# Performance work log

Measured on AMD Instinct MI355X. Metric: run time of the kernel, lower is better.

The kernel has to match this reference:

```python
import jax, jax.numpy as jnp
import numpy as np
from functools import partial

B, T, D, H, V, L, NL = 2, 2048, 512, 8, 32000, 4, 3
HID = 4 * D
HD = D // H
EPS = 1e-5


def layernorm(x, g, b):
    mu = jnp.mean(x, axis=-1, keepdims=True)
    var = jnp.mean(jnp.square(x - mu), axis=-1, keepdims=True)
    return (x - mu) * jax.lax.rsqrt(var + EPS) * g + b


def self_mod_attn(x, Wq, Wk, Wv, Wo):
    # x: [B,T,D]; W*: [D,D] (applied as x @ W)
    def heads(w):
        return jnp.transpose((x @ w).reshape(B, T, H, HD), (1, 0, 2, 3))  # [T,B,H,HD]
    q, k, v = heads(Wq), heads(Wk), heads(Wv)

    def step(mem, qkv):
        q_t, k_t, v_t = qkv  # each [B,H,HD]
        mem = mem + jnp.einsum('bhd,bhk->hdk', v_t, k_t) / B  # batch-mean outer product
        y_t = jnp.einsum('hdk,bhk->bhd', mem, q_t)
        return mem, y_t

    mem0 = jnp.zeros((H, HD, HD), dtype=x.dtype)
    _, ys = jax.lax.scan(step, mem0, (q, k, v))  # ys: [T,B,H,HD]
    out = jnp.transpose(ys, (1, 0, 2, 3)).reshape(B, T, D)
    return out @ Wo


def cms(x, W1, b1, W2, b2):
    # Continuum memory system: NL parallel MLP levels (dim -> 4*dim -> dim, GELU), averaged.
    h = jax.nn.gelu(jnp.einsum('btd,ndh->nbth', x, W1) + b1[:, None, None, :])
    y = jnp.einsum('nbth,nhd->nbtd', h, W2) + b2[:, None, None, :]
    return jnp.mean(y, axis=0)


def setup_inputs() -> dict:
    key = jax.random.key(0)
    ks = jax.random.split(key, 16)
    std = 0.02
    p = {
        'emb': jax.random.normal(ks[0], (V, D), jnp.float32) * std,
        'pos': jax.random.normal(ks[1], (2048, D), jnp.float32) * std,
        'ln1_g': jnp.ones((L, D)), 'ln1_b': jnp.zeros((L, D)),
        'Wq': jax.random.normal(ks[2], (L, D, D), jnp.float32) * std,
        'Wk': jax.random.normal(ks[3], (L, D, D), jnp.float32) * std,
        'Wv': jax.random.normal(ks[4], (L, D, D), jnp.float32) * std,
        'Wo': jax.random.normal(ks[5], (L, D, D), jnp.float32) * std,
        'ln2_g': jnp.ones((L, D)), 'ln2_b': jnp.zeros((L, D)),
        'cms_W1': jax.random.normal(ks[6], (L, NL, D, HID), jnp.float32) * std,
        'cms_b1': jnp.zeros((L, NL, HID)),
        'cms_W2': jax.random.normal(ks[7], (L, NL, HID, D), jnp.float32) * std,
        'cms_b2': jnp.zeros((L, NL, D)),
        'lnf_g': jnp.ones((D,)), 'lnf_b': jnp.zeros((D,)),
        'input_ids': jax.random.randint(ks[8], (B, T), 0, V, jnp.int32),
    }
    return p


def reference(emb, pos, ln1_g, ln1_b, Wq, Wk, Wv, Wo, ln2_g, ln2_b,
              cms_W1, cms_b1, cms_W2, cms_b2, lnf_g, lnf_b, input_ids):
    x = emb[input_ids] + pos[:T][None, :, :]  # [B,T,D]
    for l in range(L):
        x = x + self_mod_attn(layernorm(x, ln1_g[l], ln1_b[l]), Wq[l], Wk[l], Wv[l], Wo[l])
        x = x + cms(layernorm(x, ln2_g[l], ln2_b[l]), cms_W1[l], cms_b1[l], cms_W2[l], cms_b2[l])
    x = layernorm(x, lnf_g, lnf_b)
    logits = x @ emb.T  # tied head, [B,T,V]
    return logits
```

## Files before the change

### kernel.cpp

```cpp
#include <hip/hip_runtime.h>
#include <stdint.h>

#define B_ 2
#define T_ 2048
#define D_ 512
#define H_ 8
#define HD_ 64
#define V_ 32000
#define L_ 4
#define NL_ 3
#define HID_ 2048
#define NROW 4096
#define CCH 64
#define CROWS 128
#define NC 32
#define EPS_ 1e-5f

typedef __attribute__((ext_vector_type(8))) __bf16 bf16x8;
typedef __attribute__((ext_vector_type(4))) float f32x4;

__device__ __forceinline__ float b2f(unsigned short u) {
  union { uint32_t i; float f; } v; v.i = ((uint32_t)u) << 16; return v.f;
}
__device__ __forceinline__ unsigned short f2b(float f) {
  union { float f; uint32_t i; } v; v.f = f;
  uint32_t u = v.i;
  u += 0x7fffu + ((u >> 16) & 1u);
  return (unsigned short)(u >> 16);
}

__global__ __launch_bounds__(256) void k_prep(
    const float* __restrict__ emb, const float* __restrict__ pos,
    const int* __restrict__ ids,
    const float* __restrict__ Wq, const float* __restrict__ Wk,
    const float* __restrict__ Wv, const float* __restrict__ Wo,
    const float* __restrict__ W1, const float* __restrict__ W2,
    const float* __restrict__ b2,
    const float* __restrict__ ln1g, const float* __restrict__ ln1b,
    unsigned short* __restrict__ WqkvT, unsigned short* __restrict__ WoT,
    unsigned short* __restrict__ W1T, unsigned short* __restrict__ W2cat,
    unsigned short* __restrict__ embB, float* __restrict__ bsum,
    float* __restrict__ x, unsigned short* __restrict__ h) {
  int bid = blockIdx.x, tid = threadIdx.x;
  __shared__ float tile[32][33];
  __shared__ float red[4], red2[4];
  int tx = tid & 31, ty = tid >> 5;
  if (bid < 4096) {
    int z = bid >> 8, r = bid & 255;
    int bx = (r & 15) * 32, by = (r >> 4) * 32;
    const float* in; unsigned short* out;
    if (z < 12) {
      int l = z / 3, m = z - l * 3;
      in = (m == 0 ? Wq : m == 1 ? Wk : Wv) + (size_t)l * D_ * D_;
      out = WqkvT + (size_t)z * D_ * D_;
    } else {
      in = Wo + (size_t)(z - 12) * D_ * D_;
      out = WoT + (size_t)(z - 12) * D_ * D_;
    }
#pragma unroll
    for (int i = 0; i < 4; i++)
      tile[ty + 8 * i][tx] = in[(size_t)(by + ty + 8 * i) * D_ + bx + tx];
    __syncthreads();
#pragma unroll
    for (int i = 0; i < 4; i++)
      out[(size_t)(bx + ty + 8 * i) * D_ + by + tx] = f2b(tile[tx][ty + 8 * i]);
  } else if (bid < 16384) {
    int s = bid - 4096;
    int z = s >> 10, r = s & 1023;
    int bx = (r & 63) * 32, by = (r >> 6) * 32;
    const float* in = W1 + (size_t)z * D_ * HID_;
    unsigned short* out = W1T + (size_t)z * HID_ * D_;
#pragma unroll
    for (int i = 0; i < 4; i++)
      tile[ty + 8 * i][tx] = in[(size_t)(by + ty + 8 * i) * HID_ + bx + tx];
    __syncthreads();
#pragma unroll
    for (int i = 0; i < 4; i++)
      out[(size_t)(bx + ty + 8 * i) * D_ + by + tx] = f2b(tile[tx][ty + 8 * i]);
  } else if (bid < 28672) {
    int s = bid - 16384;
    int z = s >> 10, r = s & 1023;
    int l = z / 3, n = z - l * 3;
    int bx = (r & 15) * 32, by = (r >> 4) * 32;
    const float* in = W2 + (size_t)z * HID_ * D_;
#pragma unroll
    for (int i = 0; i < 4; i++)
      tile[ty + 8 * i][tx] = in[(size_t)(by + ty + 8 * i) * D_ + bx + tx];
    __syncthreads();
#pragma unroll
    for (int i = 0; i < 4; i++)
      W2cat[((size_t)l * D_ + bx + ty + 8 * i) * (NL_ * HID_) + n * HID_ + by + tx] =
          f2b(tile[tx][ty + 8 * i]);
  } else if (bid < 44672) {
    int s = bid - 28672;
    int base = (s * 256 + tid) * 4;
    float4 v = *(const float4*)(emb + base);
    unsigned short o[4] = { f2b(v.x), f2b(v.y), f2b(v.z), f2b(v.w) };
    *(uint2*)(embB + base) = *(const uint2*)o;
  } else if (bid < 46720) {
    int s = bid - 44672;
    int i = s * 256 + tid;
    int row = i >> 7, cg = i & 127;
    int t = row & (T_ - 1);
    int id = ids[row];
    float4 e = ((const float4*)(emb + (size_t)id * D_))[cg];
    float4 p = ((const float4*)(pos + (size_t)t * D_))[cg];
    float4 xv; xv.x = e.x + p.x; xv.y = e.y + p.y; xv.z = e.z + p.z; xv.w = e.w + p.w;
    ((float4*)(x + (size_t)row * D_))[cg] = xv;
    float sum = xv.x + xv.y + xv.z + xv.w;
#pragma unroll
    for (int o = 32; o >= 1; o >>= 1) sum += __shfl_xor(sum, o);
    int wv = tid >> 6;
    if ((tid & 63) == 0) red[wv] = sum;
    __syncthreads();
    int wb = (tid >> 7) * 2;
    float mu = (red[wb] + red[wb + 1]) * (1.f / D_);
    float dx = xv.x - mu, dy = xv.y - mu, dz = xv.z - mu, dw = xv.w - mu;
    float s2 = dx * dx + dy * dy + dz * dz + dw * dw;
#pragma unroll
    for (int o = 32; o >= 1; o >>= 1) s2 += __shfl_xor(s2, o);
    if ((tid & 63) == 0) red2[wv] = s2;
    __syncthreads();
    float var = (red2[wb] + red2[wb + 1]) * (1.f / D_);
    float rs = rsqrtf(var + EPS_);
    float4 gv = ((const float4*)ln1g)[cg];
    float4 bv = ((const float4*)ln1b)[cg];
    unsigned short o4[4] = { f2b(dx * rs * gv.x + bv.x), f2b(dy * rs * gv.y + bv.y),
                             f2b(dz * rs * gv.z + bv.z), f2b(dw * rs * gv.w + bv.w) };
    *(uint2*)(h + (size_t)row * D_ + cg * 4) = *(const uint2*)o4;
  } else {
    int s = bid - 46720;
    int l = s >> 1, d = (s & 1) * 256 + tid;
    float acc = 0.f;
#pragma unroll
    for (int n = 0; n < NL_; n++) acc += b2[((size_t)l * NL_ + n) * D_ + d];
    bsum[(size_t)l * D_ + d] = acc;
  }
}

__global__ __launch_bounds__(128) void k_ln(
    const float* __restrict__ x, const float* __restrict__ g,
    const float* __restrict__ b, unsigned short* __restrict__ out) {
  int row = blockIdx.x;
  int tid = threadIdx.x;
  const float* xr = x + (size_t)row * D_;
  float4 v = ((const float4*)xr)[tid];
  float s = v.x + v.y + v.z + v.w;
#pragma unroll
  for (int o = 32; o >= 1; o >>= 1) s += __shfl_xor(s, o);
  __shared__ float red[2], red2[2];
  int wv = tid >> 6;
  if ((tid & 63) == 0) red[wv] = s;
  __syncthreads();
  float mu = (red[0] + red[1]) * (1.f / D_);
  float dx = v.x - mu, dy = v.y - mu, dz = v.z - mu, dw = v.w - mu;
  float s2 = dx * dx + dy * dy + dz * dz + dw * dw;
#pragma unroll
  for (int o = 32; o >= 1; o >>= 1) s2 += __shfl_xor(s2, o);
  if ((tid & 63) == 0) red2[wv] = s2;
  __syncthreads();
  float var = (red2[0] + red2[1]) * (1.f / D_);
  float rs = rsqrtf(var + EPS_);
  float4 gv = ((const float4*)g)[tid];
  float4 bv = ((const float4*)b)[tid];
  unsigned short o4[4] = { f2b(dx * rs * gv.x + bv.x), f2b(dy * rs * gv.y + bv.y),
                           f2b(dz * rs * gv.z + bv.z), f2b(dw * rs * gv.w + bv.w) };
  *(uint2*)(out + (size_t)row * D_ + tid * 4) = *(const uint2*)o4;
}

__global__ __launch_bounds__(256) void k_cmsred_ln(
    float* __restrict__ x, const float* __restrict__ parts,
    const float* __restrict__ bsum, const float* __restrict__ g,
    const float* __restrict__ b, unsigned short* __restrict__ h) {
  int bid = blockIdx.x, tid = threadIdx.x;
  int row = bid * 2 + (tid >> 7);
  int cg = tid & 127;
  size_t base = (size_t)row * D_ + cg * 4;
  float4 xv = *(const float4*)(x + base);
  float4 p0 = *(const float4*)(parts + base);
  float4 p1 = *(const float4*)(parts + (size_t)NROW * D_ + base);
  float4 p2 = *(const float4*)(parts + 2ull * NROW * D_ + base);
  float4 bs = *(const float4*)(bsum + cg * 4);
  const float k3 = 1.f / 3.f;
  xv.x += (p0.x + p1.x + p2.x + bs.x) * k3;
  xv.y += (p0.y + p1.y + p2.y + bs.y) * k3;
  xv.z += (p0.z + p1.z + p2.z + bs.z) * k3;
  xv.w += (p0.w + p1.w + p2.w + bs.w) * k3;
  *(float4*)(x + base) = xv;
  float sum = xv.x + xv.y + xv.z + xv.w;
#pragma unroll
  for (int o = 32; o >= 1; o >>= 1) sum += __shfl_xor(sum, o);
  __shared__ float red[4], red2[4];
  int wv = tid >> 6;
  if ((tid & 63) == 0) red[wv] = sum;
  __syncthreads();
  int wb = (tid >> 7) * 2;
  float mu = (red[wb] + red[wb + 1]) * (1.f / D_);
  float dx = xv.x - mu, dy = xv.y - mu, dz = xv.z - mu, dw = xv.w - mu;
  float s2 = dx * dx + dy * dy + dz * dz + dw * dw;
#pragma unroll
  for (int o = 32; o >= 1; o >>= 1) s2 += __shfl_xor(s2, o);
  if ((tid & 63) == 0) red2[wv] = s2;
  __syncthreads();
  float var = (red2[wb] + red2[wb + 1]) * (1.f / D_);
  float rs = rsqrtf(var + EPS_);
  float4 gv = ((const float4*)g)[cg];
  float4 bv = ((const float4*)b)[cg];
  unsigned short o4[4] = { f2b(dx * rs * gv.x + bv.x), f2b(dy * rs * gv.y + bv.y),
                           f2b(dz * rs * gv.z + bv.z), f2b(dw * rs * gv.w + bv.w) };
  *(uint2*)(h + base) = *(const uint2*)o4;
}

enum { E_QKV = 0, E_RES = 1, E_GELU = 2, E_PART = 3, E_F32 = 4 };

template <int TR, int NW>
__device__ __forceinline__ void stage_tile(
    const unsigned short* __restrict__ gbase, int ldk, unsigned short* lds,
    int wave, int lane) {
#pragma unroll
  for (int q = 0; q < 4; q++) {
    int Lb = (q * NW + wave) << 10;
    int L = Lb + lane * 16;
    int row = L >> 7;
    int colb = (L & 127) ^ ((row & 7) << 4);
    const unsigned short* gsrc = gbase + (size_t)row * ldk + (colb >> 1);
    __builtin_amdgcn_global_load_lds(
        (const __attribute__((address_space(1))) uint32_t*)gsrc,
        (__attribute__((address_space(3))) uint32_t*)(lds + (Lb >> 1)),
        16, 0, 0);
  }
}

template <int EPI>
__global__ __launch_bounds__(256, 2) void k_gemm128(
    const unsigned short* __restrict__ A,
    const unsigned short* __restrict__ Bt,
    const float* __restrict__ bias,
    void* __restrict__ Out,
    int Kext, int ldk, int N, int ldOut) {
  int z = blockIdx.z;
  A  += (size_t)z * Kext;
  Bt += (size_t)z * Kext;
  int lane = threadIdx.x & 63, wave = threadIdx.x >> 6;
  int wm = wave >> 1, wn = wave & 1;
  int bx = blockIdx.x, by = blockIdx.y;

  __shared__ __align__(16) unsigned short As[2][128 * 64];
  __shared__ __align__(16) unsigned short Bs[2][128 * 64];

  const unsigned short* Ab = A + (size_t)by * 128 * ldk;
  const unsigned short* Bb = Bt + (size_t)bx * 128 * ldk;

  f32x4 acc[4][4] = {};
  int nk = Kext / 64;
  stage_tile<128, 4>(Ab, ldk, As[0], wave, lane);
  stage_tile<128, 4>(Bb, ldk, Bs[0], wave, lane);
  __syncthreads();
  for (int kt = 0; kt < nk; kt++) {
    int cur = kt & 1;
    if (kt + 1 < nk) {
      stage_tile<128, 4>(Ab + (size_t)(kt + 1) * 64, ldk, As[cur ^ 1], wave, lane);
      stage_tile<128, 4>(Bb + (size_t)(kt + 1) * 64, ldk, Bs[cur ^ 1], wave, lane);
    }
    const char* Ac = (const char*)As[cur];
    const char* Bc = (const char*)Bs[cur];
#pragma unroll
    for (int kk = 0; kk < 2; kk++) {
      bf16x8 af[4], bfr[4];
#pragma unroll
      for (int mt = 0; mt < 4; mt++) {
        int row = wm * 64 + mt * 16 + (lane & 15);
        int off = ((row << 7) | (kk * 64 + ((lane >> 4) << 4))) ^ ((row & 7) << 4);
        af[mt] = *(const bf16x8*)(Ac + off);
      }
#pragma unroll
      for (int nt = 0; nt < 4; nt++) {
        int row = wn * 64 + nt * 16 + (lane & 15);
        int off = ((row << 7) | (kk * 64 + ((lane >> 4) << 4))) ^ ((row & 7) << 4);
        bfr[nt] = *(const bf16x8*)(Bc + off);
      }
#pragma unroll
      for (int mt = 0; mt < 4; mt++)
#pragma unroll
        for (int nt = 0; nt < 4; nt++)
          acc[mt][nt] = __builtin_amdgcn_mfma_f32_16x16x32_bf16(
              af[mt], bfr[nt], acc[mt][nt], 0, 0, 0);
    }
    __syncthreads();
  }

  int gm = by * 128 + wm * 64;
  int gn = bx * 128 + wn * 64;
#pragma unroll
  for (int mt = 0; mt < 4; mt++) {
#pragma unroll
    for (int nt = 0; nt < 4; nt++) {
      int m0 = gm + mt * 16 + ((lane >> 4) << 2);
      int n = gn + nt * 16 + (lane & 15);
#pragma unroll
      for (int j = 0; j < 4; j++) {
        float v = acc[mt][nt][j];
        int m = m0 + j;
        if constexpr (EPI == E_QKV) {
          int zq = n >> 9, col = n & 511;
          ((unsigned short*)Out)[((size_t)zq * NROW + m) * D_ + col] = f2b(v);
        } else if constexpr (EPI == E_RES) {
          size_t idx = (size_t)m * ldOut + n;
          ((float*)Out)[idx] = bias[idx] + v;
        } else if constexpr (EPI == E_GELU) {
          size_t idx = (size_t)m * ldOut + n;
          v += bias[n];
          float u2 = 1.5957691216057308f * (v + 0.044715f * v * v * v);
          float sg = 1.f / (1.f + __expf(-u2));
          ((unsigned short*)Out)[idx] = f2b(v * sg);
        } else {
          ((float*)Out)[(size_t)z * NROW * D_ + (size_t)m * ldOut + n] = v;
        }
      }
    }
  }
}

__global__ __launch_bounds__(512) void k_gemm256(
    const unsigned short* __restrict__ A,
    const unsigned short* __restrict__ Bt,
    void* __restrict__ Out,
    int K, int N, int ldOut) {
  int lane = threadIdx.x & 63, wave = threadIdx.x >> 6;
  int wm = wave >> 2, wn = wave & 3;
  int lin = blockIdx.y * 125 + blockIdx.x;
  int seg = lin / 400, rem = lin % 400;
  int bx = seg * 25 + rem % 25, by = rem / 25;

  __shared__ __align__(16) unsigned short As[256 * 64];
  __shared__ __align__(16) unsigned short Bs[256 * 64];

  const unsigned short* Ab = A + (size_t)by * 256 * K;
  const unsigned short* Bb = Bt + (size_t)bx * 256 * K;

  f32x4 acc[8][4] = {};
  int nk = K / 64;
  for (int kt = 0; kt < nk; kt++) {
    stage_tile<256, 8>(Ab + (size_t)kt * 64, K, As, wave, lane);
    stage_tile<256, 8>(Bb + (size_t)kt * 64, K, Bs, wave, lane);
    __syncthreads();
    const char* Ac = (const char*)As;
    const char* Bc = (const char*)Bs;
#pragma unroll
    for (int kk = 0; kk < 2; kk++) {
      bf16x8 af[8], bfr[4];
#pragma unroll
      for (int mt = 0; mt < 8; mt++) {
        int row = wm * 128 + mt * 16 + (lane & 15);
        int off = ((row << 7) | (kk * 64 + ((lane >> 4) << 4))) ^ ((row & 7) << 4);
        af[mt] = *(const bf16x8*)(Ac + off);
      }
#pragma unroll
      for (int nt = 0; nt < 4; nt++) {
        int row = wn * 64 + nt * 16 + (lane & 15);
        int off = ((row << 7) | (kk * 64 + ((lane >> 4) << 4))) ^ ((row & 7) << 4);
        bfr[nt] = *(const bf16x8*)(Bc + off);
      }
#pragma unroll
      for (int mt = 0; mt < 8; mt++)
#pragma unroll
        for (int nt = 0; nt < 4; nt++)
          acc[mt][nt] = __builtin_amdgcn_mfma_f32_16x16x32_bf16(
              af[mt], bfr[nt], acc[mt][nt], 0, 0, 0);
    }
    __syncthreads();
  }

  int gm = by * 256 + wm * 128;
  int gn = bx * 256 + wn * 64;
#pragma unroll
  for (int mt = 0; mt < 8; mt++) {
#pragma unroll
    for (int nt = 0; nt < 4; nt++) {
      int m0 = gm + mt * 16 + ((lane >> 4) << 2);
      int n = gn + nt * 16 + (lane & 15);
#pragma unroll
      for (int j = 0; j < 4; j++)
        ((float*)Out)[(size_t)(m0 + j) * ldOut + n] = acc[mt][nt][j];
    }
  }
}

__device__ __forceinline__ void unpack8f(uint4 u, float* dst) {
  dst[0] = b2f((unsigned short)(u.x & 0xffff)); dst[1] = b2f((unsigned short)(u.x >> 16));
  dst[2] = b2f((unsigned short)(u.y & 0xffff)); dst[3] = b2f((unsigned short)(u.y >> 16));
  dst[4] = b2f((unsigned short)(u.z & 0xffff)); dst[5] = b2f((unsigned short)(u.z >> 16));
  dst[6] = b2f((unsigned short)(u.w & 0xffff)); dst[7] = b2f((unsigned short)(u.w >> 16));
}

__global__ __launch_bounds__(256) void k_attnA(
    const unsigned short* __restrict__ kbuf, const unsigned short* __restrict__ vbuf,
    float* __restrict__ G) {
  int c = blockIdx.x, h = blockIdx.y;
  __shared__ __align__(16) float Ks[CROWS][HD_];
  __shared__ __align__(16) float Vs[CROWS][HD_];
  int tid = threadIdx.x;
#pragma unroll
  for (int it = 0; it < 4; it++) {
    int gi = it * 256 + tid;
    int r = gi >> 3, c8 = gi & 7;
    int bb = r & 1, tt = c * CCH + (r >> 1);
    size_t goff = ((size_t)bb * T_ + tt) * D_ + h * HD_ + c8 * 8;
    uint4 kv = *(const uint4*)(kbuf + goff);
    uint4 vv = *(const uint4*)(vbuf + goff);
    unpack8f(kv, &Ks[r][c8 * 8]);
    unpack8f(vv, &Vs[r][c8 * 8]);
  }
  __syncthreads();
  int d = tid & 63, kb = (tid >> 6) * 16;
  float acc[16] = {};
  for (int r = 0; r < CROWS; r++) {
    float vd = Vs[r][d];
#pragma unroll
    for (int j = 0; j < 16; j++) acc[j] += vd * Ks[r][kb + j];
  }
  float* Gp = G + (((size_t)c * H_ + h) * HD_ + d) * HD_ + kb;
#pragma unroll
  for (int j = 0; j < 16; j++) Gp[j] = 0.5f * acc[j];
}

__global__ __launch_bounds__(256) void k_attnB(const float* __restrict__ G,
                                               float* __restrict__ Mem) {
  int hh = blockIdx.x >> 4, seg = blockIdx.x & 15;
  int idx = seg * 256 + threadIdx.x;
  float g[NC];
#pragma unroll
  for (int c = 0; c < NC; c++)
    g[c] = G[((size_t)c * H_ + hh) * (HD_ * HD_) + idx];
  float m = 0.f;
#pragma unroll
  for (int c = 0; c < NC; c++) {
    Mem[((size_t)c * H_ + hh) * (HD_ * HD_) + idx] = m;
    m += g[c];
  }
}

__global__ __launch_bounds__(256) void k_attnC(
    const unsigned short* __restrict__ qbuf, const unsigned short* __restrict__ kbuf,
    const unsigned short* __restrict__ vbuf, const float* __restrict__ Mem,
    unsigned short* __restrict__ ybuf) {
  int c = blockIdx.x, h = blockIdx.y;
  __shared__ __align__(16) unsigned short smem[32768];
  unsigned short* Qs  = smem;
  unsigned short* Ksh = smem + 8192;
  unsigned short* Vt  = smem + 16384;
  unsigned short* Mhi = smem + 24576;
  unsigned short* Mlo = smem + 28672;
  unsigned short* Ps  = smem;

  int tid = threadIdx.x, lane = tid & 63, w = tid >> 6;
#pragma unroll
  for (int it = 0; it < 4; it++) {
    int gi = it * 256 + tid;
    int r = gi >> 3, g8 = gi & 7;
    int bb = r & 1, tt = c * CCH + (r >> 1);
    size_t go = ((size_t)bb * T_ + tt) * D_ + h * HD_ + g8 * 8;
    int qc = (g8 * 8) ^ ((r & 7) << 3);
    *(uint4*)(Qs + r * 64 + qc) = *(const uint4*)(qbuf + go);
    *(uint4*)(Ksh + r * 64 + qc) = *(const uint4*)(kbuf + go);
    uint4 vv = *(const uint4*)(vbuf + go);
    const unsigned short* vp = (const unsigned short*)&vv;
#pragma unroll
    for (int j = 0; j < 8; j++) {
      int d = g8 * 8 + j;
      int t = (d & 7) ^ (d >> 3);
      Vt[d * 128 + (r ^ (t << 3))] = vp[j];
    }
  }
  {
    const float* Mp = Mem + (((size_t)c * H_ + h) << 12);
#pragma unroll
    for (int it = 0; it < 16; it++) {
      int i = it * 256 + tid;
      int d = i >> 6, k = i & 63;
      float m = Mp[i];
      unsigned short hi = f2b(m);
      float lo = m - b2f(hi);
      int col = k ^ ((d & 7) << 3);
      Mhi[d * 64 + col] = hi;
      Mlo[d * 64 + col] = f2b(lo);
    }
  }
  __syncthreads();

  int row0 = w * 32;
  f32x4 sacc[2][8] = {};
  f32x4 yacc[2][4] = {};
#pragma unroll
  for (int kk = 0; kk < 2; kk++) {
    bf16x8 aq[2];
#pragma unroll
    for (int mt = 0; mt < 2; mt++) {
      int row = row0 + mt * 16 + (lane & 15);
      aq[mt] = *(const bf16x8*)(Qs + row * 64 +
                ((kk * 32 + ((lane >> 4) << 3)) ^ ((row & 7) << 3)));
    }
#pragma unroll
    for (int nt = 0; nt < 8; nt++) {
      int row = nt * 16 + (lane & 15);
      bf16x8 bk = *(const bf16x8*)(Ksh + row * 64 +
                ((kk * 32 + ((lane >> 4) << 3)) ^ ((row & 7) << 3)));
#pragma unroll
      for (int mt = 0; mt < 2; mt++)
        sacc[mt][nt] = __builtin_amdgcn_mfma_f32_16x16x32_bf16(aq[mt], bk,
                                                               sacc[mt][nt], 0, 0, 0);
    }
#pragma unroll
    for (int nt = 0; nt < 4; nt++) {
      int row = nt * 16 + (lane & 15);
      int off = row * 64 + ((kk * 32 + ((lane >> 4) << 3)) ^ ((row & 7) << 3));
      bf16x8 bh = *(const bf16x8*)(Mhi + off);
      bf16x8 bl = *(const bf16x8*)(Mlo + off);
#pragma unroll
      for (int mt = 0; mt < 2; mt++) {
        yacc[mt][nt] = __builtin_amdgcn_mfma_f32_16x16x32_bf16(aq[mt], bh,
                                                               yacc[mt][nt], 0, 0, 0);
        yacc[mt][nt] = __builtin_amdgcn_mfma_f32_16x16x32_bf16(aq[mt], bl,
                                                               yacc[mt][nt], 0, 0, 0);
      }
    }
  }
  __syncthreads();

#pragma unroll
  for (int mt = 0; mt < 2; mt++)
#pragma unroll
    for (int nt = 0; nt < 8; nt++)
#pragma unroll
      for (int j = 0; j < 4; j++) {
        int qr = row0 + mt * 16 + ((lane >> 4) << 2) + j;
        int ks = nt * 16 + (lane & 15);
        float v = ((ks >> 1) <= (qr >> 1)) ? sacc[mt][nt][j] * 0.5f : 0.f;
        Ps[qr * 128 + (ks ^ ((qr & 7) << 3))] = f2b(v);
      }
  __syncthreads();

  for (int kb = 0; kb <= w; kb++) {
    bf16x8 ap[2];
#pragma unroll
    for (int mt = 0; mt < 2; mt++) {
      int row = row0 + mt * 16 + (lane & 15);
      ap[mt] = *(const bf16x8*)(Ps + row * 128 +
                ((kb * 32 + ((lane >> 4) << 3)) ^ ((row & 7) << 3)));
    }
#pragma unroll
    for (int nt = 0; nt < 4; nt++) {
      int d = nt * 16 + (lane & 15);
      int t = (d & 7) ^ (d >> 3);
      int gb = (kb * 32 + ((lane >> 4) << 3)) ^ (t << 3);
      bf16x8 bv = *(const bf16x8*)(Vt + d * 128 + gb);
#pragma unroll
      for (int mt = 0; mt < 2; mt++)
        yacc[mt][nt] = __builtin_amdgcn_mfma_f32_16x16x32_bf16(ap[mt], bv,
                                                               yacc[mt][nt], 0, 0, 0);
    }
  }

#pragma unroll
  for (int mt = 0; mt < 2; mt++)
#pragma unroll
    for (int nt = 0; nt < 4; nt++)
#pragma unroll
      for (int j = 0; j < 4; j++) {
        int qr = row0 + mt * 16 + ((lane >> 4) << 2) + j;
        int d = nt * 16 + (lane & 15);
        int bb = qr & 1, tl = qr >> 1;
        ybuf[((size_t)bb * T_ + c * CCH + tl) * D_ + h * HD_ + d] =
            f2b(yacc[mt][nt][j]);
      }
}

extern "C" void kernel_launch(void* const* d_in, const int* in_sizes, int n_in,
                              void* d_out, int out_size, void* d_ws, size_t ws_size,
                              hipStream_t stream) {
  (void)in_sizes; (void)n_in; (void)out_size; (void)ws_size;
  const float* emb  = (const float*)d_in[0];
  const float* pos  = (const float*)d_in[1];
  const float* ln1g = (const float*)d_in[2];
  const float* ln1b = (const float*)d_in[3];
  const float* Wq   = (const float*)d_in[4];
  const float* Wk   = (const float*)d_in[5];
  const float* Wv   = (const float*)d_in[6];
  const float* Wo   = (const float*)d_in[7];
  const float* ln2g = (const float*)d_in[8];
  const float* ln2b = (const float*)d_in[9];
  const float* W1   = (const float*)d_in[10];
  const float* b1   = (const float*)d_in[11];
  const float* W2   = (const float*)d_in[12];
  const float* b2   = (const float*)d_in[13];
  const float* lnfg = (const float*)d_in[14];
  const float* lnfb = (const float*)d_in[15];
  const int*   ids  = (const int*)d_in[16];

  char* w = (char*)d_ws;
  size_t off = 0;
  auto alloc = [&](size_t bytes) -> void* {
    void* p = w + off; off += (bytes + 255) & ~(size_t)255; return p;
  };
  const size_t DD = (size_t)D_ * D_;
  unsigned short* WqkvT = (unsigned short*)alloc(12ull * DD * 2);
  unsigned short* WoT   = (unsigned short*)alloc(4ull * DD * 2);
  unsigned short* W1T   = (unsigned short*)alloc((size_t)L_ * NL_ * HID_ * D_ * 2);
  unsigned short* W2cat = (unsigned short*)alloc((size_t)L_ * D_ * NL_ * HID_ * 2);
  unsigned short* embB  = (unsigned short*)alloc((size_t)V_ * D_ * 2);
  float* bsum           = (float*)alloc((size_t)L_ * D_ * 4);
  float* x              = (float*)alloc((size_t)NROW * D_ * 4);
  unsigned short* h     = (unsigned short*)alloc((size_t)NROW * D_ * 2);
  unsigned short* qkv   = (unsigned short*)alloc(3ull * NROW * D_ * 2);
  unsigned short* ybuf  = (unsigned short*)alloc((size_t)NROW * D_ * 2);
  float* G              = (float*)alloc((size_t)NC * H_ * HD_ * HD_ * 4);
  float* Mem            = (float*)alloc((size_t)NC * H_ * HD_ * HD_ * 4);
  float* parts          = (float*)qkv;
  unsigned short* hmid  = (unsigned short*)alloc((size_t)NROW * NL_ * HID_ * 2);

  dim3 blk(256);
  k_prep<<<dim3(46728), blk, 0, stream>>>(emb, pos, ids, Wq, Wk, Wv, Wo, W1, W2, b2,
                                          ln1g, ln1b,
                                          WqkvT, WoT, W1T, W2cat, embB, bsum, x, h);

  unsigned short* qb = qkv;
  unsigned short* kb = qkv + (size_t)NROW * D_;
  unsigned short* vb = qkv + 2ull * NROW * D_;

  for (int l = 0; l < L_; l++) {
    k_gemm128<E_QKV><<<dim3(12, 32), blk, 0, stream>>>(
        h, WqkvT + (size_t)l * 3 * DD, bsum, qkv, D_, D_, 3 * D_, D_);
    k_attnA<<<dim3(NC, H_), blk, 0, stream>>>(kb, vb, G);
    k_attnB<<<dim3(H_ * 16), blk, 0, stream>>>(G, Mem);
    k_attnC<<<dim3(NC, H_), blk, 0, stream>>>(qb, kb, vb, Mem, ybuf);
    k_gemm128<E_RES><<<dim3(4, 32), blk, 0, stream>>>(
        ybuf, WoT + (size_t)l * DD, x, x, D_, D_, D_, D_);
    k_ln<<<dim3(NROW), dim3(128), 0, stream>>>(x, ln2g + l * D_, ln2b + l * D_, h);
    k_gemm128<E_GELU><<<dim3(48, 32), blk, 0, stream>>>(
        h, W1T + (size_t)l * NL_ * HID_ * D_, b1 + (size_t)l * NL_ * HID_, hmid,
        D_, D_, NL_ * HID_, NL_ * HID_);
    k_gemm128<E_PART><<<dim3(4, 32, 3), blk, 0, stream>>>(
        hmid, W2cat + (size_t)l * D_ * NL_ * HID_, bsum, parts,
        2048, NL_ * HID_, D_, D_);
    const float* gn = (l < 3) ? (ln1g + (l + 1) * D_) : lnfg;
    const float* bn = (l < 3) ? (ln1b + (l + 1) * D_) : lnfb;
    k_cmsred_ln<<<dim3(NROW / 2), blk, 0, stream>>>(x, parts, bsum + l * D_, gn, bn, h);
  }
  k_gemm256<<<dim3(125, 16), dim3(512), 0, stream>>>(h, embB, d_out, D_, V_, V_);
}
```

Baseline: 919.2 us.

## Double-buffer 256-tile GEMM, use it for GELU GEMM, fold prefix-sum into attnC

The 256x256 GEMM now double-buffers its LDS tiles so the global loads for the next K-slice overlap the MFMA work on the current one. It is templated and also used for the CMS up-projection with the GELU epilogue, replacing the 128-tile kernel there. The separate prefix-sum kernel (attnB) is removed and each attnC block sums the earlier chunk outer products itself, saving a launch and the Mem round trip at the cost of redundant reads. attnA's inner loop is also rewritten to use float4 LDS reads; doubled LDS lowers occupancy to one block per CU.

Result: slower. 972.8 us (+5.8%).

```diff
diff --git a/kernel.cpp b/kernel.cpp
--- a/kernel.cpp
+++ b/kernel.cpp
@@ -307,81 +307,95 @@
         } else if constexpr (EPI == E_RES) {
           size_t idx = (size_t)m * ldOut + n;
           ((float*)Out)[idx] = bias[idx] + v;
-        } else if constexpr (EPI == E_GELU) {
-          size_t idx = (size_t)m * ldOut + n;
+        } else {
+          ((float*)Out)[(size_t)z * NROW * D_ + (size_t)m * ldOut + n] = v;
+        }
+      }
+    }
+  }
+}
+
+template <int EPI>
+__global__ __launch_bounds__(512, 1) void k_gemm256(
+    const unsigned short* __restrict__ A,
+    const unsigned short* __restrict__ Bt,
+    const float* __restrict__ bias,
+    void* __restrict__ Out,
+    int K, int N, int ldOut) {
+  int lane = threadIdx.x & 63, wave = threadIdx.x >> 6;
+  int wm = wave >> 2, wn = wave & 3;
+  int bx = blockIdx.x, by = blockIdx.y;
+  if constexpr (EPI == E_F32) {
+    int lin = blockIdx.y * 125 + blockIdx.x;
+    int seg = lin / 400, rem = lin % 400;
+    bx = seg * 25 + rem % 25;  by = rem / 25;
+  }
+
+  __shared__ __align__(16) unsigned short As[2][256 * 64];
+  __shared__ __align__(16) unsigned short Bs[2][256 * 64];
+
+  const unsigned short* Ab = A + (size_t)by * 256 * K;
+  const unsigned short* Bb = Bt + (size_t)bx * 256 * K;
+
+  f32x4 acc[8][4] = {};
+  int nk = K / 64;
+  stage_tile<256, 8>(Ab, K, As[0], wave, lane);
+  stage_tile<256, 8>(Bb, K, Bs[0], wave, lane);
+  __syncthreads();
+  for (int kt = 0; kt < nk; kt++) {
+    int cur = kt & 1;
+    if (kt + 1 < nk) {
+      stage_tile<256, 8>(Ab + (size_t)(kt + 1) * 64, K, As[cur ^ 1], wave, lane);
+      stage_tile<256, 8>(Bb + (size_t)(kt + 1) * 64, K, Bs[cur ^ 1], wave, lane);
+    }
+    const char* Ac = (const char*)As[cur];
+    const char* Bc = (const char*)Bs[cur];
+#pragma unroll
+    for (int kk = 0; kk < 2; kk++) {
+      bf16x8 af[8], bfr[4];
+#pragma unroll
+      for (int mt = 0; mt < 8; mt++) {
+        int row = wm * 128 + mt * 16 + (lane & 15);
+        int off = ((row << 7) | (kk * 64 + ((lane >> 4) << 4))) ^ ((row & 7) << 4);
+        af[mt] = *(const bf16x8*)(Ac + off);
+      }
+#pragma unroll
+      for (int nt = 0; nt < 4; nt++) {
+        int row = wn * 64 + nt * 16 + (lane & 15);
+        int off = ((row << 7) | (kk * 64 + ((lane >> 4) << 4))) ^ ((row & 7) << 4);
+        bfr[nt] = *(const bf16x8*)(Bc + off);
+      }
+#pragma unroll
+      for (int mt = 0; mt < 8; mt++)
+#pragma unroll
+        for (int nt = 0; nt < 4; nt++)
+          acc[mt][nt] = __builtin_amdgcn_mfma_f32_16x16x32_bf16(
+              af[mt], bfr[nt], acc[mt][nt], 0, 0, 0);
+    }
+    __syncthreads();
+  }
+
+  int gm = by * 256 + wm * 128;
+  int gn = bx * 256 + wn * 64;
+#pragma unroll
+  for (int mt = 0; mt < 8; mt++) {
+#pragma unroll
+    for (int nt = 0; nt < 4; nt++) {
+      int m0 = gm + mt * 16 + ((lane >> 4) << 2);
+      int n = gn + nt * 16 + (lane & 15);
+#pragma unroll
+      for (int j = 0; j < 4; j++) {
+        float v = acc[mt][nt][j];
+        size_t idx = (size_t)(m0 + j) * ldOut + n;
+        if constexpr (EPI == E_GELU) {
           v += bias[n];
           float u2 = 1.5957691216057308f * (v + 0.044715f * v * v * v);
           float sg = 1.f / (1.f + __expf(-u2));
           ((unsigned short*)Out)[idx] = f2b(v * sg);
         } else {
-          ((float*)Out)[(size_t)z * NROW * D_ + (size_t)m * ldOut + n] = v;
+          ((float*)Out)[idx] = v;
         }
       }
-    }
-  }
-}
-
-__global__ __launch_bounds__(512) void k_gemm256(
-    const unsigned short* __restrict__ A,
-    const unsigned short* __restrict__ Bt,
-    void* __restrict__ Out,
-    int K, int N, int ldOut) {
-  int lane = threadIdx.x & 63, wave = threadIdx.x >> 6;
-  int wm = wave >> 2, wn = wave & 3;
-  int lin = blockIdx.y * 125 + blockIdx.x;
-  int seg = lin / 400, rem = lin % 400;
-  int bx = seg * 25 + rem % 25, by = rem / 25;
-
-  __shared__ __align__(16) unsigned short As[256 * 64];
-  __shared__ __align__(16) unsigned short Bs[256 * 64];
-
-  const unsigned short* Ab = A + (size_t)by * 256 * K;
-  const unsigned short* Bb = Bt + (size_t)bx * 256 * K;
-
-  f32x4 acc[8][4] = {};
-  int nk = K / 64;
-  for (int kt = 0; kt < nk; kt++) {
-    stage_tile<256, 8>(Ab + (size_t)kt * 64, K, As, wave, lane);
-    stage_tile<256, 8>(Bb + (size_t)kt * 64, K, Bs, wave, lane);
-    __syncthreads();
-    const char* Ac = (const char*)As;
-    const char* Bc = (const char*)Bs;
-#pragma unroll
-    for (int kk = 0; kk < 2; kk++) {
-      bf16x8 af[8], bfr[4];
-#pragma unroll
-      for (int mt = 0; mt < 8; mt++) {
-        int row = wm * 128 + mt * 16 + (lane & 15);
-        int off = ((row << 7) | (kk * 64 + ((lane >> 4) << 4))) ^ ((row & 7) << 4);
-        af[mt] = *(const bf16x8*)(Ac + off);
-      }
-#pragma unroll
-      for (int nt = 0; nt < 4; nt++) {
-        int row = wn * 64 + nt * 16 + (lane & 15);
-        int off = ((row << 7) | (kk * 64 + ((lane >> 4) << 4))) ^ ((row & 7) << 4);
-        bfr[nt] = *(const bf16x8*)(Bc + off);
-      }
-#pragma unroll
-      for (int mt = 0; mt < 8; mt++)
-#pragma unroll
-        for (int nt = 0; nt < 4; nt++)
-          acc[mt][nt] = __builtin_amdgcn_mfma_f32_16x16x32_bf16(
-              af[mt], bfr[nt], acc[mt][nt], 0, 0, 0);
-    }
-    __syncthreads();
-  }
-
-  int gm = by * 256 + wm * 128;
-  int gn = bx * 256 + wn * 64;
-#pragma unroll
-  for (int mt = 0; mt < 8; mt++) {
-#pragma unroll
-    for (int nt = 0; nt < 4; nt++) {
-      int m0 = gm + mt * 16 + ((lane >> 4) << 2);
-      int n = gn + nt * 16 + (lane & 15);
-#pragma unroll
-      for (int j = 0; j < 4; j++)
-        ((float*)Out)[(size_t)(m0 + j) * ldOut + n] = acc[mt][nt][j];
     }
   }
 }
@@ -416,33 +430,21 @@
   float acc[16] = {};
   for (int r = 0; r < CROWS; r++) {
     float vd = Vs[r][d];
-#pragma unroll
-    for (int j = 0; j < 16; j++) acc[j] += vd * Ks[r][kb + j];
+    const float4* Kr = (const float4*)(&Ks[r][kb]);
+    float4 k0 = Kr[0], k1 = Kr[1], k2 = Kr[2], k3 = Kr[3];
+    acc[0] += vd * k0.x;  acc[1] += vd * k0.y;  acc[2] += vd * k0.z;  acc[3] += vd * k0.w;
+    acc[4] += vd * k1.x;  acc[5] += vd * k1.y;  acc[6] += vd * k1.z;  acc[7] += vd * k1.w;
+    acc[8] += vd * k2.x;  acc[9] += vd * k2.y;  acc[10] += vd * k2.z; acc[11] += vd * k2.w;
+    acc[12] += vd * k3.x; acc[13] += vd * k3.y; acc[14] += vd * k3.z; acc[15] += vd * k3.w;
   }
   float* Gp = G + (((size_t)c * H_ + h) * HD_ + d) * HD_ + kb;
 #pragma unroll
   for (int j = 0; j < 16; j++) Gp[j] = 0.5f * acc[j];
-}
-
-__global__ __launch_bounds__(256) void k_attnB(const float* __restrict__ G,
-                                               float* __restrict__ Mem) {
-  int hh = blockIdx.x >> 4, seg = blockIdx.x & 15;
-  int idx = seg * 256 + threadIdx.x;
-  float g[NC];
-#pragma unroll
-  for (int c = 0; c < NC; c++)
-    g[c] = G[((size_t)c * H_ + hh) * (HD_ * HD_) + idx];
-  float m = 0.f;
-#pragma unroll
-  for (int c = 0; c < NC; c++) {
-    Mem[((size_t)c * H_ + hh) * (HD_ * HD_) + idx] = m;
-    m += g[c];
-  }
 }
 
 __global__ __launch_bounds__(256) void k_attnC(
     const unsigned short* __restrict__ qbuf, const unsigned short* __restrict__ kbuf,
-    const unsigned short* __restrict__ vbuf, const float* __restrict__ Mem,
+    const unsigned short* __restrict__ vbuf, const float* __restrict__ G,
     unsigned short* __restrict__ ybuf) {
   int c = blockIdx.x, h = blockIdx.y;
   __shared__ __align__(16) unsigned short smem[32768];
@@ -454,6 +456,18 @@
   unsigned short* Ps  = smem;
 
   int tid = threadIdx.x, lane = tid & 63, w = tid >> 6;
+  float macc[16] = {};
+  for (int cp = 0; cp < c; cp++) {
+    const float4* gp = (const float4*)(G + ((size_t)cp * H_ + h) * (HD_ * HD_)) + tid * 4;
+#pragma unroll
+    for (int j4 = 0; j4 < 4; j4++) {
+      float4 gv = gp[j4];
+      macc[j4 * 4]     += gv.x;
+      macc[j4 * 4 + 1] += gv.y;
+      macc[j4 * 4 + 2] += gv.z;
+      macc[j4 * 4 + 3] += gv.w;
+    }
+  }
 #pragma unroll
   for (int it = 0; it < 4; it++) {
     int gi = it * 256 + tid;
@@ -472,19 +486,15 @@
       Vt[d * 128 + (r ^ (t << 3))] = vp[j];
     }
   }
-  {
-    const float* Mp = Mem + (((size_t)c * H_ + h) << 12);
-#pragma unroll
-    for (int it = 0; it < 16; it++) {
-      int i = it * 256 + tid;
-      int d = i >> 6, k = i & 63;
-      float m = Mp[i];
-      unsigned short hi = f2b(m);
-      float lo = m - b2f(hi);
-      int col = k ^ ((d & 7) << 3);
-      Mhi[d * 64 + col] = hi;
-      Mlo[d * 64 + col] = f2b(lo);
-    }
+#pragma unroll
+  for (int j = 0; j < 16; j++) {
+    int i = tid * 16 + j;
+    int d = i >> 6, k = i & 63;
+    unsigned short hi = f2b(macc[j]);
+    float lo = macc[j] - b2f(hi);
+    int col = k ^ ((d & 7) << 3);
+    Mhi[d * 64 + col] = hi;
+    Mlo[d * 64 + col] = f2b(lo);
   }
   __syncthreads();
 
@@ -614,7 +624,7 @@
   unsigned short* qkv   = (unsigned short*)alloc(3ull * NROW * D_ * 2);
   unsigned short* ybuf  = (unsigned short*)alloc((size_t)NROW * D_ * 2);
   float* G              = (float*)alloc((size_t)NC * H_ * HD_ * HD_ * 4);
-  float* Mem            = (float*)alloc((size_t)NC * H_ * HD_ * HD_ * 4);
+  (void)alloc((size_t)NC * H_ * HD_ * HD_ * 4);
   float* parts          = (float*)qkv;
   unsigned short* hmid  = (unsigned short*)alloc((size_t)NROW * NL_ * HID_ * 2);
 
@@ -631,14 +641,13 @@
     k_gemm128<E_QKV><<<dim3(12, 32), blk, 0, stream>>>(
         h, WqkvT + (size_t)l * 3 * DD, bsum, qkv, D_, D_, 3 * D_, D_);
     k_attnA<<<dim3(NC, H_), blk, 0, stream>>>(kb, vb, G);
-    k_attnB<<<dim3(H_ * 16), blk, 0, stream>>>(G, Mem);
-    k_attnC<<<dim3(NC, H_), blk, 0, stream>>>(qb, kb, vb, Mem, ybuf);
+    k_attnC<<<dim3(NC, H_), blk, 0, stream>>>(qb, kb, vb, G, ybuf);
     k_gemm128<E_RES><<<dim3(4, 32), blk, 0, stream>>>(
         ybuf, WoT + (size_t)l * DD, x, x, D_, D_, D_, D_);
     k_ln<<<dim3(NROW), dim3(128), 0, stream>>>(x, ln2g + l * D_, ln2b + l * D_, h);
-    k_gemm128<E_GELU><<<dim3(48, 32), blk, 0, stream>>>(
+    k_gemm256<E_GELU><<<dim3(24, 16), dim3(512), 0, stream>>>(
         h, W1T + (size_t)l * NL_ * HID_ * D_, b1 + (size_t)l * NL_ * HID_, hmid,
-        D_, D_, NL_ * HID_, NL_ * HID_);
+        D_, NL_ * HID_, NL_ * HID_);
     k_gemm128<E_PART><<<dim3(4, 32, 3), blk, 0, stream>>>(
         hmid, W2cat + (size_t)l * D_ * NL_ * HID_, bsum, parts,
         2048, NL_ * HID_, D_, D_);
@@ -646,5 +655,6 @@
     const float* bn = (l < 3) ? (ln1b + (l + 1) * D_) : lnfb;
     k_cmsred_ln<<<dim3(NROW / 2), blk, 0, stream>>>(x, parts, bsum + l * D_, gn, bn, h);
   }
-  k_gemm256<<<dim3(125, 16), dim3(512), 0, stream>>>(h, embB, d_out, D_, V_, V_);
-}
+  k_gemm256<E_F32><<<dim3(125, 16), dim3(512), 0, stream>>>(
+      h, embB, bsum, d_out, D_, V_, V_);
+}
```
